# Kernel tuning notes

Hardware: AMD Instinct MI355X
Metric: run time of the kernel (lower is better)

## Reference

```python
import jax, jax.numpy as jnp
import numpy as np

N = 100000      # nodes
E = 1000000     # edges
G = 1024        # graphs
NODE_IN, CLIMBER_IN, HID, OUT, HEADS = 6, 4, 64, 4, 2
SLOPE = 0.2     # PyG GATConv default negative_slope


def gat_conv(x, edge_index, W, att_src, att_dst, bias):
    """PyG GATConv, heads=HEADS, concat=False (mean over heads), add_self_loops=True."""
    heads, ch = att_src.shape
    xp = (x @ W).reshape(-1, heads, ch)                       # [N,H,C]
    a_src = jnp.einsum('nhc,hc->nh', xp, att_src)             # [N,H]
    a_dst = jnp.einsum('nhc,hc->nh', xp, att_dst)
    loops = jnp.arange(x.shape[0])
    src = jnp.concatenate([edge_index[0], loops])             # [E+N]
    dst = jnp.concatenate([edge_index[1], loops])
    e = jax.nn.leaky_relu(a_src[src] + a_dst[dst], SLOPE)     # [E+N,H]
    emax = jax.ops.segment_max(e, dst, num_segments=x.shape[0])
    emax = jnp.where(jnp.isfinite(emax), emax, 0.0)
    ex = jnp.exp(e - emax[dst])
    den = jax.ops.segment_sum(ex, dst, num_segments=x.shape[0])
    alpha = ex / (den[dst] + 1e-16)                           # segment softmax over incoming edges
    msg = xp[src] * alpha[:, :, None]                         # [E+N,H,C]
    agg = jax.ops.segment_sum(msg, dst, num_segments=x.shape[0])  # [N,H,C]
    return agg.mean(axis=1) + bias                            # concat=False -> head mean


def setup_inputs() -> dict:
    key = jax.random.key(0)
    ks = jax.random.split(key, 20)
    s = lambda *d: 1.0 / np.sqrt(d[0])
    inp = {
        'x': jax.random.normal(ks[0], (N, NODE_IN), jnp.float32),
        'edge_index': jax.random.randint(ks[1], (2, E), 0, N),
        'batch': jnp.sort(jax.random.randint(ks[2], (N,), 0, G)),
        'climber': jax.random.normal(ks[3], (G, CLIMBER_IN), jnp.float32),
        # conv1 params
        'W1': jax.random.normal(ks[4], (NODE_IN, HEADS * HID), jnp.float32) * s(NODE_IN),
        'as1': jax.random.normal(ks[5], (HEADS, HID), jnp.float32) * s(HID),
        'ad1': jax.random.normal(ks[6], (HEADS, HID), jnp.float32) * s(HID),
        'b1': jnp.zeros((HID,), jnp.float32),
        # conv2 params
        'W2': jax.random.normal(ks[7], (HID, HEADS * HID), jnp.float32) * s(HID),
        'as2': jax.random.normal(ks[8], (HEADS, HID), jnp.float32) * s(HID),
        'ad2': jax.random.normal(ks[9], (HEADS, HID), jnp.float32) * s(HID),
        'b2': jnp.zeros((HID,), jnp.float32),
        # climber embed
        'Wc': jax.random.normal(ks[10], (CLIMBER_IN, HID), jnp.float32) * s(CLIMBER_IN),
        'bc': jnp.zeros((HID,), jnp.float32),
        # classifier
        'Wm1': jax.random.normal(ks[11], (2 * HID, HID), jnp.float32) * s(2 * HID),
        'bm1': jnp.zeros((HID,), jnp.float32),
        'Wm2': jax.random.normal(ks[12], (HID, OUT), jnp.float32) * s(HID),
        'bm2': jnp.zeros((OUT,), jnp.float32),
    }
    return inp


def reference(x, edge_index, batch, climber, W1, as1, ad1, b1, W2, as2, ad2, b2,
              Wc, bc, Wm1, bm1, Wm2, bm2):
    h = jax.nn.relu(gat_conv(x, edge_index, W1, as1, ad1, b1))
    h = jax.nn.relu(gat_conv(h, edge_index, W2, as2, ad2, b2))
    c = jax.nn.relu(climber @ Wc + bc)            # dropout is identity in eval mode
    z = jnp.concatenate([h, c[batch]], axis=1)    # [N, 2*HID]
    z = jax.nn.relu(z @ Wm1 + bm1)                # dropout identity (eval)
    return z @ Wm2 + bm2                          # [N, OUT]
```

## Files before the change

### kernel.cpp

```cpp
#include <hip/hip_runtime.h>
#include <hip/hip_fp16.h>

#define SLOPE 0.2f

__device__ __forceinline__ float lrelu(float v) { return v >= 0.f ? v : SLOPE * v; }

__device__ __forceinline__ unsigned pack2(float a, float b) {
    __half2 h = __floats2half2_rn(a, b);
    return *reinterpret_cast<unsigned*>(&h);
}

__device__ __forceinline__ void mix8(float4& A, float4& B, float a, uint4 u) {
    asm("v_fma_mix_f32 %0, %8, %12, %0 op_sel:[0,0,0] op_sel_hi:[1,0,0]\n\t"
        "v_fma_mix_f32 %1, %8, %12, %1 op_sel:[1,0,0] op_sel_hi:[1,0,0]\n\t"
        "v_fma_mix_f32 %2, %9, %12, %2 op_sel:[0,0,0] op_sel_hi:[1,0,0]\n\t"
        "v_fma_mix_f32 %3, %9, %12, %3 op_sel:[1,0,0] op_sel_hi:[1,0,0]\n\t"
        "v_fma_mix_f32 %4, %10, %12, %4 op_sel:[0,0,0] op_sel_hi:[1,0,0]\n\t"
        "v_fma_mix_f32 %5, %10, %12, %5 op_sel:[1,0,0] op_sel_hi:[1,0,0]\n\t"
        "v_fma_mix_f32 %6, %11, %12, %6 op_sel:[0,0,0] op_sel_hi:[1,0,0]\n\t"
        "v_fma_mix_f32 %7, %11, %12, %7 op_sel:[1,0,0] op_sel_hi:[1,0,0]"
        : "+v"(A.x), "+v"(A.y), "+v"(A.z), "+v"(A.w),
          "+v"(B.x), "+v"(B.y), "+v"(B.z), "+v"(B.w)
        : "v"(u.x), "v"(u.y), "v"(u.z), "v"(u.w), "v"(a));
}

template <int K>
__global__ __launch_bounds__(256)
void k_xp_gemm(const float* __restrict__ x, const float* __restrict__ W,
               const float* __restrict__ as_, const float* __restrict__ ad_,
               __half* __restrict__ xph, float* __restrict__ asrc,
               float* __restrict__ adst, int N) {
    constexpr int ZS = K + 1;
    __shared__ float zs[64 * ZS];
    __shared__ float ws[K * 128];
    const int n0 = blockIdx.x * 64;
    const int t = threadIdx.x;

    for (int i = t; i < K * 32; i += 256) ((float4*)ws)[i] = ((const float4*)W)[i];
    if constexpr (K % 4 == 0) {
        constexpr int K4 = K / 4;
        for (int i = t; i < 64 * K4; i += 256) {
            int n = i / K4, k4 = i - n * K4;
            int gn = n0 + n;
            float4 v = (gn < N) ? ((const float4*)x)[(size_t)gn * K4 + k4]
                                : make_float4(0.f, 0.f, 0.f, 0.f);
            float* zr = zs + n * ZS + k4 * 4;
            zr[0] = v.x; zr[1] = v.y; zr[2] = v.z; zr[3] = v.w;
        }
    } else {
        for (int i = t; i < 64 * K; i += 256) {
            int n = i / K, k = i - n * K;
            int gn = n0 + n;
            zs[n * ZS + k] = (gn < N) ? x[(size_t)gn * K + k] : 0.f;
        }
    }
    __syncthreads();

    const int tx = t & 15, ty = t >> 4;
    const int c0a = tx * 4;
    const int c0b = 64 + tx * 4;

    float4 asA = *(const float4*)(as_ + c0a);
    float4 asB = *(const float4*)(as_ + c0b);
    float4 adA = *(const float4*)(ad_ + c0a);
    float4 adB = *(const float4*)(ad_ + c0b);

    float acc[4][8];
    #pragma unroll
    for (int i = 0; i < 4; ++i)
        #pragma unroll
        for (int j = 0; j < 8; ++j) acc[i][j] = 0.f;

    for (int k = 0; k < K; ++k) {
        float4 w0 = *(const float4*)(ws + k * 128 + c0a);
        float4 w1 = *(const float4*)(ws + k * 128 + c0b);
        #pragma unroll
        for (int i = 0; i < 4; ++i) {
            float zv = zs[(ty * 4 + i) * ZS + k];
            acc[i][0] += zv * w0.x; acc[i][1] += zv * w0.y;
            acc[i][2] += zv * w0.z; acc[i][3] += zv * w0.w;
            acc[i][4] += zv * w1.x; acc[i][5] += zv * w1.y;
            acc[i][6] += zv * w1.z; acc[i][7] += zv * w1.w;
        }
    }

    #pragma unroll
    for (int i = 0; i < 4; ++i) {
        int nl = ty * 4 + i, gn = n0 + nl;
        if (gn < N) {
            uint2 ua, ub;
            ua.x = pack2(acc[i][0], acc[i][1]);
            ua.y = pack2(acc[i][2], acc[i][3]);
            ub.x = pack2(acc[i][4], acc[i][5]);
            ub.y = pack2(acc[i][6], acc[i][7]);
            *(uint2*)(xph + (size_t)gn * 128 + c0a) = ua;
            *(uint2*)(xph + (size_t)gn * 128 + c0b) = ub;
        }
        float ps0 = acc[i][0]*asA.x + acc[i][1]*asA.y + acc[i][2]*asA.z + acc[i][3]*asA.w;
        float ps1 = acc[i][4]*asB.x + acc[i][5]*asB.y + acc[i][6]*asB.z + acc[i][7]*asB.w;
        float pd0 = acc[i][0]*adA.x + acc[i][1]*adA.y + acc[i][2]*adA.z + acc[i][3]*adA.w;
        float pd1 = acc[i][4]*adB.x + acc[i][5]*adB.y + acc[i][6]*adB.z + acc[i][7]*adB.w;
        #pragma unroll
        for (int off = 1; off <= 8; off <<= 1) {
            ps0 += __shfl_xor(ps0, off, 64);
            ps1 += __shfl_xor(ps1, off, 64);
            pd0 += __shfl_xor(pd0, off, 64);
            pd1 += __shfl_xor(pd1, off, 64);
        }
        if (tx == 0 && gn < N) {
            asrc[gn * 2]     = ps0;
            asrc[gn * 2 + 1] = ps1;
            adst[gn * 2]     = pd0;
            adst[gn * 2 + 1] = pd1;
        }
    }
}

__global__ void k_hist(const int* __restrict__ dst, int* __restrict__ deg,
                       int* __restrict__ rank, int E) {
    int e = blockIdx.x * blockDim.x + threadIdx.x;
    if (e < E) rank[e] = atomicAdd(&deg[dst[e]], 1);
}

__global__ void k_scan_partial(const int* __restrict__ deg, int* __restrict__ partial, int N) {
    int b = blockIdx.x, t = threadIdx.x;
    int base = b * 1024 + t * 4;
    int s = 0;
    for (int i = 0; i < 4; ++i) { int idx = base + i; if (idx < N) s += deg[idx]; }
    __shared__ int sh[256];
    sh[t] = s; __syncthreads();
    for (int off = 128; off > 0; off >>= 1) { if (t < off) sh[t] += sh[t + off]; __syncthreads(); }
    if (t == 0) partial[b] = sh[0];
}

__global__ void k_scan_final(const int* __restrict__ deg, const int* __restrict__ partial,
                             int* __restrict__ rowptr, int N, int E, int nb) {
    int b = blockIdx.x, t = threadIdx.x;
    __shared__ int shp[256];
    shp[t] = (t < nb) ? partial[t] : 0;
    __syncthreads();
    for (int off = 1; off < 256; off <<= 1) {
        int v = (t >= off) ? shp[t - off] : 0;
        __syncthreads();
        shp[t] += v;
        __syncthreads();
    }
    int pbase = (b > 0) ? shp[b - 1] : 0;
    __syncthreads();

    int base = b * 1024 + t * 4;
    int local[4]; int s = 0;
    for (int i = 0; i < 4; ++i) { int idx = base + i; local[i] = (idx < N) ? deg[idx] : 0; s += local[i]; }
    __shared__ int sh[256];
    int orig = s;
    sh[t] = s; __syncthreads();
    for (int off = 1; off < 256; off <<= 1) {
        int v = (t >= off) ? sh[t - off] : 0;
        __syncthreads();
        sh[t] += v;
        __syncthreads();
    }
    int run = pbase + sh[t] - orig;
    for (int i = 0; i < 4; ++i) {
        int idx = base + i;
        if (idx < N) rowptr[idx] = run;
        run += local[i];
    }
    if (b == 0 && t == 0) rowptr[N] = E;
}

__global__ void k_scatter(const int* __restrict__ src, const int* __restrict__ dst,
                          const int* __restrict__ rowptr, const int* __restrict__ rank,
                          int* __restrict__ csr_src, int E) {
    int e = blockIdx.x * blockDim.x + threadIdx.x;
    if (e >= E) return;
    int d = dst[e];
    csr_src[rowptr[d] + rank[e]] = src[e];
}

__global__ void k_ag(const int* __restrict__ rowptr, const int* __restrict__ csr_src,
                     const float* __restrict__ asrc, const float* __restrict__ adst,
                     const __half* __restrict__ xph, const float* __restrict__ b,
                     float* __restrict__ hout, int N) {
    int tid = blockIdx.x * blockDim.x + threadIdx.x;
    int lane = threadIdx.x & 63;
    int wid = tid >> 6;
    int nw = (gridDim.x * blockDim.x) >> 6;
    const int l  = lane & 31;
    const int hh = lane >> 5;
    const int g4 = (lane >> 3) & 3;
    const int c8 = lane & 7;
    const int lofs = hh * 8 + c8;
    const uint4* xp4 = (const uint4*)xph;
    float4 bb0 = ((const float4*)b)[c8 * 2];
    float4 bb1 = ((const float4*)b)[c8 * 2 + 1];

    for (int n = wid; n < N; n += nw) {
        int rs = rowptr[n], re = rowptr[n + 1], cnt = re - rs;
        uint4 uself = xp4[(size_t)n * 16 + lofs];
        float a_dst = adst[n * 2 + hh];
        float eself = __expf(lrelu(asrc[n * 2 + hh] + a_dst));

        float4 accA = make_float4(0.f, 0.f, 0.f, 0.f);
        float4 accB = make_float4(0.f, 0.f, 0.f, 0.f);
        float den;

        if (cnt <= 32) {
            float ev = 0.f; int s_reg = n;
            if (l < cnt) {
                s_reg = csr_src[rs + l];
                ev = __expf(lrelu(asrc[s_reg * 2 + hh] + a_dst));
            }
            if (g4 == 0) mix8(accA, accB, eself, uself);

            const int base = (hh << 5) - rs;
            int e0 = rs;
            for (; e0 + 4 < re; e0 += 8) {
                int ea = e0 + g4, eb = e0 + 4 + g4;
                float aa = __shfl(ev,    base + ea, 64);
                int   sa = __shfl(s_reg, base + ea, 64);
                float ab = __shfl(ev,    base + eb, 64);
                int   sb = __shfl(s_reg, base + eb, 64);
                if (eb >= re) { ab = 0.f; sb = n; }
                uint4 u1 = xp4[(size_t)sa * 16 + lofs];
                uint4 u2 = xp4[(size_t)sb * 16 + lofs];
                mix8(accA, accB, aa, u1);
                mix8(accA, accB, ab, u2);
            }
            if (e0 < re) {
                int ea = e0 + g4;
                float aa = __shfl(ev,    base + ea, 64);
                int   sa = __shfl(s_reg, base + ea, 64);
                if (ea >= re) { aa = 0.f; sa = n; }
                uint4 u1 = xp4[(size_t)sa * 16 + lofs];
                mix8(accA, accB, aa, u1);
            }
            den = ev + (l == 0 ? eself : 0.f);
            #pragma unroll
            for (int off = 16; off > 0; off >>= 1) den += __shfl_xor(den, off, 64);
        } else {
            den = (l == 0) ? eself : 0.f;
            for (int e = rs + l; e < re; e += 32)
                den += __expf(lrelu(asrc[csr_src[e] * 2 + hh] + a_dst));
            #pragma unroll
            for (int off = 16; off > 0; off >>= 1) den += __shfl_xor(den, off, 64);
            if (g4 == 0) mix8(accA, accB, eself, uself);
            for (int e0 = rs; e0 < re; e0 += 8) {
                int ea = e0 + g4, eb = e0 + 4 + g4;
                bool va = ea < re, vb = eb < re;
                int sa = va ? csr_src[ea] : n;
                int sb = vb ? csr_src[eb] : n;
                float aa = va ? __expf(lrelu(asrc[sa * 2 + hh] + a_dst)) : 0.f;
                float ab = vb ? __expf(lrelu(asrc[sb * 2 + hh] + a_dst)) : 0.f;
                uint4 u1 = xp4[(size_t)sa * 16 + lofs];
                uint4 u2 = xp4[(size_t)sb * 16 + lofs];
                mix8(accA, accB, aa, u1);
                mix8(accA, accB, ab, u2);
            }
        }

        float inv = 1.f / (den + 1e-16f);

        #pragma unroll
        for (int off = 8; off <= 16; off <<= 1) {
            accA.x += __shfl_xor(accA.x, off, 64);
            accA.y += __shfl_xor(accA.y, off, 64);
            accA.z += __shfl_xor(accA.z, off, 64);
            accA.w += __shfl_xor(accA.w, off, 64);
            accB.x += __shfl_xor(accB.x, off, 64);
            accB.y += __shfl_xor(accB.y, off, 64);
            accB.z += __shfl_xor(accB.z, off, 64);
            accB.w += __shfl_xor(accB.w, off, 64);
        }
        accA.x *= inv; accA.y *= inv; accA.z *= inv; accA.w *= inv;
        accB.x *= inv; accB.y *= inv; accB.z *= inv; accB.w *= inv;
        accA.x += __shfl_xor(accA.x, 32, 64);
        accA.y += __shfl_xor(accA.y, 32, 64);
        accA.z += __shfl_xor(accA.z, 32, 64);
        accA.w += __shfl_xor(accA.w, 32, 64);
        accB.x += __shfl_xor(accB.x, 32, 64);
        accB.y += __shfl_xor(accB.y, 32, 64);
        accB.z += __shfl_xor(accB.z, 32, 64);
        accB.w += __shfl_xor(accB.w, 32, 64);

        if (lane < 8) {
            float4 r0, r1;
            r0.x = fmaxf(accA.x * 0.5f + bb0.x, 0.f);
            r0.y = fmaxf(accA.y * 0.5f + bb0.y, 0.f);
            r0.z = fmaxf(accA.z * 0.5f + bb0.z, 0.f);
            r0.w = fmaxf(accA.w * 0.5f + bb0.w, 0.f);
            r1.x = fmaxf(accB.x * 0.5f + bb1.x, 0.f);
            r1.y = fmaxf(accB.y * 0.5f + bb1.y, 0.f);
            r1.z = fmaxf(accB.z * 0.5f + bb1.z, 0.f);
            r1.w = fmaxf(accB.w * 0.5f + bb1.w, 0.f);
            ((float4*)hout)[(size_t)n * 16 + c8 * 2]     = r0;
            ((float4*)hout)[(size_t)n * 16 + c8 * 2 + 1] = r1;
        }
    }
}

__global__ __launch_bounds__(256)
void k_climber_cpre(const float* __restrict__ climber, const float* __restrict__ Wc,
                    const float* __restrict__ bc, const float* __restrict__ Wm1,
                    const float* __restrict__ bm1, float* __restrict__ cpre, int G) {
    __shared__ float ce[4][64];
    __shared__ float wm1b[64 * 64];
    int t = threadIdx.x;
    for (int i = t; i < 1024; i += 256) ((float4*)wm1b)[i] = ((const float4*)Wm1)[1024 + i];
    int gl = t >> 6, c = t & 63;
    int g = blockIdx.x * 4 + gl;
    float acc = bc[c];
    if (g < G)
        for (int k = 0; k < 4; ++k) acc += climber[g * 4 + k] * Wc[k * 64 + c];
    ce[gl][c] = fmaxf(acc, 0.f);
    __syncthreads();
    float o = bm1[c];
    for (int k = 0; k < 64; ++k) o += ce[gl][k] * wm1b[k * 64 + c];
    if (g < G) cpre[(size_t)g * 64 + c] = o;
}

__global__ __launch_bounds__(256)
void k_final(const float* __restrict__ h2, const float* __restrict__ cpre,
             const int* __restrict__ batch, const float* __restrict__ Wm1,
             const float* __restrict__ Wm2, const float* __restrict__ bm2,
             float* __restrict__ out, int N) {
    __shared__ float zs[64 * 65];
    __shared__ float ws[64 * 64];
    __shared__ float4 w2l[64];
    const int n0 = blockIdx.x * 64;
    const int t = threadIdx.x;

    for (int i = t; i < 1024; i += 256) ((float4*)ws)[i] = ((const float4*)Wm1)[i];
    if (t < 64) w2l[t] = ((const float4*)Wm2)[t];
    for (int i = t; i < 64 * 16; i += 256) {
        int n = i >> 4, k4 = i & 15;
        int gn = n0 + n;
        float4 v = (gn < N) ? ((const float4*)h2)[(size_t)gn * 16 + k4]
                            : make_float4(0.f, 0.f, 0.f, 0.f);
        float* zr = zs + n * 65 + k4 * 4;
        zr[0] = v.x; zr[1] = v.y; zr[2] = v.z; zr[3] = v.w;
    }
    __syncthreads();

    const int tx = t & 15, ty = t >> 4;
    const int c0 = tx * 4;
    float acc[4][4];
    #pragma unroll
    for (int i = 0; i < 4; ++i)
        #pragma unroll
        for (int j = 0; j < 4; ++j) acc[i][j] = 0.f;

    for (int k = 0; k < 64; ++k) {
        float4 wv = *(const float4*)(ws + k * 64 + c0);
        #pragma unroll
        for (int i = 0; i < 4; ++i) {
            float zv = zs[(ty * 4 + i) * 65 + k];
            acc[i][0] += zv * wv.x; acc[i][1] += zv * wv.y;
            acc[i][2] += zv * wv.z; acc[i][3] += zv * wv.w;
        }
    }
    __syncthreads();

    float4 wa = w2l[c0], wb = w2l[c0 + 1], wc = w2l[c0 + 2], wd = w2l[c0 + 3];
    #pragma unroll
    for (int i = 0; i < 4; ++i) {
        int nl = ty * 4 + i, gn = n0 + nl;
        float4 o = make_float4(0.f, 0.f, 0.f, 0.f);
        if (gn < N) {
            int b = batch[gn];
            float4 cp = *(const float4*)(cpre + (size_t)b * 64 + c0);
            float m0 = fmaxf(acc[i][0] + cp.x, 0.f);
            float m1 = fmaxf(acc[i][1] + cp.y, 0.f);
            float m2 = fmaxf(acc[i][2] + cp.z, 0.f);
            float m3 = fmaxf(acc[i][3] + cp.w, 0.f);
            o.x = m0 * wa.x + m1 * wb.x + m2 * wc.x + m3 * wd.x;
            o.y = m0 * wa.y + m1 * wb.y + m2 * wc.y + m3 * wd.y;
            o.z = m0 * wa.z + m1 * wb.z + m2 * wc.z + m3 * wd.z;
            o.w = m0 * wa.w + m1 * wb.w + m2 * wc.w + m3 * wd.w;
        }
        *(float4*)(zs + tx * 260 + nl * 4) = o;
    }
    __syncthreads();
    {
        int nl = t >> 2, j = t & 3, gn = n0 + nl;
        float s = 0.f;
        #pragma unroll
        for (int tx2 = 0; tx2 < 16; ++tx2) s += zs[tx2 * 260 + nl * 4 + j];
        if (gn < N) out[(size_t)gn * 4 + j] = s + bm2[j];
    }
}

extern "C" void kernel_launch(void* const* d_in, const int* in_sizes, int n_in,
                              void* d_out, int out_size, void* d_ws, size_t ws_size,
                              hipStream_t stream) {
    const float* x       = (const float*)d_in[0];
    const int*   ei      = (const int*)  d_in[1];
    const int*   batch   = (const int*)  d_in[2];
    const float* climber = (const float*)d_in[3];
    const float* W1  = (const float*)d_in[4];
    const float* as1 = (const float*)d_in[5];
    const float* ad1 = (const float*)d_in[6];
    const float* b1  = (const float*)d_in[7];
    const float* W2  = (const float*)d_in[8];
    const float* as2 = (const float*)d_in[9];
    const float* ad2 = (const float*)d_in[10];
    const float* b2  = (const float*)d_in[11];
    const float* Wc  = (const float*)d_in[12];
    const float* bc  = (const float*)d_in[13];
    const float* Wm1 = (const float*)d_in[14];
    const float* bm1 = (const float*)d_in[15];
    const float* Wm2 = (const float*)d_in[16];
    const float* bm2 = (const float*)d_in[17];

    const int N  = in_sizes[0] / 6;
    const int E  = in_sizes[1] / 2;
    const int G  = in_sizes[3] / 4;

    const int* srcI = ei;
    const int* dstI = ei + E;

    char* base = (char*)d_ws;
    size_t off = 0;
    auto carve = [&](size_t bytes) { void* p = base + off; off += (bytes + 255) & ~size_t(255); return p; };
    __half* xph   = (__half*)carve((size_t)N * 128 * 2);
    float* hbuf   = (float*)carve((size_t)N * 64 * 4);
    float* asrc   = (float*)carve((size_t)N * 2 * 4);
    float* adst   = (float*)carve((size_t)N * 2 * 4);
    float* cpre   = (float*)carve((size_t)G * 64 * 4);
    int*   deg    = (int*)  carve((size_t)N * 4);
    int*   rowptr = (int*)  carve((size_t)(N + 1) * 4);
    int*   rank   = (int*)  carve((size_t)E * 4);
    int*   partial= (int*)  carve(4096 * 4);
    int*   csr_src= (int*)  carve((size_t)E * 4);

    const int tpb = 256;
    const int nScanBlk = (N + 1023) / 1024;
    const int nEdgeBlk = (E + tpb - 1) / tpb;
    const int PG = 2048;
    const int nTile = (N + 63) / 64;

    hipMemsetAsync(deg, 0, (size_t)N * 4, stream);
    k_hist<<<nEdgeBlk, tpb, 0, stream>>>(dstI, deg, rank, E);
    k_scan_partial<<<nScanBlk, tpb, 0, stream>>>(deg, partial, N);
    k_scan_final<<<nScanBlk, tpb, 0, stream>>>(deg, partial, rowptr, N, E, nScanBlk);
    k_scatter<<<nEdgeBlk, tpb, 0, stream>>>(srcI, dstI, rowptr, rank, csr_src, E);

    k_xp_gemm<6><<<nTile, tpb, 0, stream>>>(x, W1, as1, ad1, xph, asrc, adst, N);
    k_ag<<<PG, tpb, 0, stream>>>(rowptr, csr_src, asrc, adst, xph, b1, hbuf, N);

    k_xp_gemm<64><<<nTile, tpb, 0, stream>>>(hbuf, W2, as2, ad2, xph, asrc, adst, N);
    k_ag<<<PG, tpb, 0, stream>>>(rowptr, csr_src, asrc, adst, xph, b2, hbuf, N);

    k_climber_cpre<<<(G + 3) / 4, tpb, 0, stream>>>(climber, Wc, bc, Wm1, bm1, cpre, G);
    k_final<<<nTile, tpb, 0, stream>>>(hbuf, cpre, batch, Wm1, Wm2, bm2, (float*)d_out, N);
}
```

Measured before the change: 330.0 us.

## Software-pipeline per-node loads in GAT aggregation with contiguous node chunks

The aggregation kernel now gives each wavefront a contiguous chunk of nodes instead of a grid-strided set. It loads the chunk's row pointers once across lanes and reads them back with shuffles. While the current node is being aggregated, it prefetches the next node's CSR indices, self features and attention scalars, and loads the next node's source attention values after the current gather. The aim is to hide the dependent load latency at the start of each node, at the cost of more live registers and some load imbalance between wavefronts with different chunk contents.

```diff
diff --git a/kernel.cpp b/kernel.cpp
--- a/kernel.cpp
+++ b/kernel.cpp
@@ -195,32 +195,67 @@
     float4 bb0 = ((const float4*)b)[c8 * 2];
     float4 bb1 = ((const float4*)b)[c8 * 2 + 1];
 
-    for (int n = wid; n < N; n += nw) {
-        int rs = rowptr[n], re = rowptr[n + 1], cnt = re - rs;
-        uint4 uself = xp4[(size_t)n * 16 + lofs];
-        float a_dst = adst[n * 2 + hh];
-        float eself = __expf(lrelu(asrc[n * 2 + hh] + a_dst));
-
+    const int cpw = (N + nw - 1) / nw;
+    const int nb = wid * cpw;
+    if (nb >= N) return;
+    const int ne = min(N, nb + cpw);
+    const bool use_rp = (cpw <= 62);
+
+    int rpv = 0;
+    if (use_rp) {
+        int gi = nb + lane;
+        rpv = (gi <= ne) ? rowptr[gi] : 0;
+    }
+
+    int rs, re;
+    if (use_rp) { rs = __shfl(rpv, 0, 64); re = __shfl(rpv, 1, 64); }
+    else        { rs = rowptr[nb];         re = rowptr[nb + 1]; }
+    int cnt = re - rs;
+    int   s_cur = nb;
+    float a_cur = 0.f;
+    if (cnt <= 32 && l < cnt) {
+        s_cur = csr_src[rs + l];
+        a_cur = asrc[s_cur * 2 + hh];
+    }
+    uint4 u_self = xp4[(size_t)nb * 16 + lofs];
+    float asel   = asrc[nb * 2 + hh];
+    float adv    = adst[nb * 2 + hh];
+
+    for (int n = nb; n < ne; ++n) {
+        const int i = n - nb;
+        const int n1 = n + 1;
+        const bool has1 = n1 < ne;
+
+        int rs1 = 0, re1 = 0, cnt1 = 0, s_nxt = n1;
+        uint4 u_nxt = make_uint4(0u, 0u, 0u, 0u);
+        float asel_nxt = 0.f, adv_nxt = 0.f;
+        if (has1) {
+            if (use_rp) { rs1 = __shfl(rpv, i + 1, 64); re1 = __shfl(rpv, i + 2, 64); }
+            else        { rs1 = rowptr[n1];             re1 = rowptr[n1 + 1]; }
+            cnt1 = re1 - rs1;
+            if (cnt1 <= 32 && l < cnt1) s_nxt = csr_src[rs1 + l];
+            u_nxt    = xp4[(size_t)n1 * 16 + lofs];
+            asel_nxt = asrc[n1 * 2 + hh];
+            adv_nxt  = adst[n1 * 2 + hh];
+        }
+
+        float eself = __expf(lrelu(asel + adv));
         float4 accA = make_float4(0.f, 0.f, 0.f, 0.f);
         float4 accB = make_float4(0.f, 0.f, 0.f, 0.f);
         float den;
 
         if (cnt <= 32) {
-            float ev = 0.f; int s_reg = n;
-            if (l < cnt) {
-                s_reg = csr_src[rs + l];
-                ev = __expf(lrelu(asrc[s_reg * 2 + hh] + a_dst));
-            }
-            if (g4 == 0) mix8(accA, accB, eself, uself);
+            float ev = (l < cnt) ? __expf(lrelu(a_cur + adv)) : 0.f;
+            if (g4 == 0) mix8(accA, accB, eself, u_self);
 
             const int base = (hh << 5) - rs;
             int e0 = rs;
             for (; e0 + 4 < re; e0 += 8) {
                 int ea = e0 + g4, eb = e0 + 4 + g4;
                 float aa = __shfl(ev,    base + ea, 64);
-                int   sa = __shfl(s_reg, base + ea, 64);
+                int   sa = __shfl(s_cur, base + ea, 64);
                 float ab = __shfl(ev,    base + eb, 64);
-                int   sb = __shfl(s_reg, base + eb, 64);
+                int   sb = __shfl(s_cur, base + eb, 64);
                 if (eb >= re) { ab = 0.f; sb = n; }
                 uint4 u1 = xp4[(size_t)sa * 16 + lofs];
                 uint4 u2 = xp4[(size_t)sb * 16 + lofs];
@@ -230,7 +265,7 @@
             if (e0 < re) {
                 int ea = e0 + g4;
                 float aa = __shfl(ev,    base + ea, 64);
-                int   sa = __shfl(s_reg, base + ea, 64);
+                int   sa = __shfl(s_cur, base + ea, 64);
                 if (ea >= re) { aa = 0.f; sa = n; }
                 uint4 u1 = xp4[(size_t)sa * 16 + lofs];
                 mix8(accA, accB, aa, u1);
@@ -241,23 +276,26 @@
         } else {
             den = (l == 0) ? eself : 0.f;
             for (int e = rs + l; e < re; e += 32)
-                den += __expf(lrelu(asrc[csr_src[e] * 2 + hh] + a_dst));
+                den += __expf(lrelu(asrc[csr_src[e] * 2 + hh] + adv));
             #pragma unroll
             for (int off = 16; off > 0; off >>= 1) den += __shfl_xor(den, off, 64);
-            if (g4 == 0) mix8(accA, accB, eself, uself);
+            if (g4 == 0) mix8(accA, accB, eself, u_self);
             for (int e0 = rs; e0 < re; e0 += 8) {
                 int ea = e0 + g4, eb = e0 + 4 + g4;
                 bool va = ea < re, vb = eb < re;
                 int sa = va ? csr_src[ea] : n;
                 int sb = vb ? csr_src[eb] : n;
-                float aa = va ? __expf(lrelu(asrc[sa * 2 + hh] + a_dst)) : 0.f;
-                float ab = vb ? __expf(lrelu(asrc[sb * 2 + hh] + a_dst)) : 0.f;
+                float aa = va ? __expf(lrelu(asrc[sa * 2 + hh] + adv)) : 0.f;
+                float ab = vb ? __expf(lrelu(asrc[sb * 2 + hh] + adv)) : 0.f;
                 uint4 u1 = xp4[(size_t)sa * 16 + lofs];
                 uint4 u2 = xp4[(size_t)sb * 16 + lofs];
                 mix8(accA, accB, aa, u1);
                 mix8(accA, accB, ab, u2);
             }
         }
+
+        float a_nxt = 0.f;
+        if (has1 && cnt1 <= 32 && l < cnt1) a_nxt = asrc[s_nxt * 2 + hh];
 
         float inv = 1.f / (den + 1e-16f);
 
@@ -296,6 +334,10 @@
             ((float4*)hout)[(size_t)n * 16 + c8 * 2]     = r0;
             ((float4*)hout)[(size_t)n * 16 + c8 * 2 + 1] = r1;
         }
+
+        rs = rs1; re = re1; cnt = cnt1;
+        s_cur = s_nxt; a_cur = a_nxt;
+        u_self = u_nxt; asel = asel_nxt; adv = adv_nxt;
     }
 }
 
```

After: 367.8 us. 1.11x slower.

## Fuse scatter, layer-1 projection and climber kernels; store hidden activations in fp16

Applied to the files above, without the earlier changes.

Merges the CSR scatter, the first-layer projection GEMM and the climber precompute into one launch, dispatching on block index, so three independent kernels run concurrently and two launches disappear. The intermediate hidden buffer between layers is now stored as fp16 instead of fp32, which halves its write and read traffic in the aggregation, second GEMM and final kernels. The cost is reduced precision on the hidden activations and a larger, branchier fused kernel whose shared-memory footprint is sized for the largest branch.

```diff
diff --git a/kernel.cpp b/kernel.cpp
--- a/kernel.cpp
+++ b/kernel.cpp
@@ -8,6 +8,10 @@
 __device__ __forceinline__ unsigned pack2(float a, float b) {
     __half2 h = __floats2half2_rn(a, b);
     return *reinterpret_cast<unsigned*>(&h);
+}
+__device__ __forceinline__ float2 h2f(unsigned u) {
+    __half2 h = *reinterpret_cast<__half2*>(&u);
+    return __half22float2(h);
 }
 
 __device__ __forceinline__ void mix8(float4& A, float4& B, float a, uint4 u) {
@@ -24,12 +28,12 @@
         : "v"(u.x), "v"(u.y), "v"(u.z), "v"(u.w), "v"(a));
 }
 
-template <int K>
 __global__ __launch_bounds__(256)
-void k_xp_gemm(const float* __restrict__ x, const float* __restrict__ W,
-               const float* __restrict__ as_, const float* __restrict__ ad_,
-               __half* __restrict__ xph, float* __restrict__ asrc,
-               float* __restrict__ adst, int N) {
+void k_xp_gemm64h(const __half* __restrict__ x, const float* __restrict__ W,
+                  const float* __restrict__ as_, const float* __restrict__ ad_,
+                  __half* __restrict__ xph, float* __restrict__ asrc,
+                  float* __restrict__ adst, int N) {
+    constexpr int K = 64;
     constexpr int ZS = K + 1;
     __shared__ float zs[64 * ZS];
     __shared__ float ws[K * 128];
@@ -37,22 +41,15 @@
     const int t = threadIdx.x;
 
     for (int i = t; i < K * 32; i += 256) ((float4*)ws)[i] = ((const float4*)W)[i];
-    if constexpr (K % 4 == 0) {
-        constexpr int K4 = K / 4;
-        for (int i = t; i < 64 * K4; i += 256) {
-            int n = i / K4, k4 = i - n * K4;
-            int gn = n0 + n;
-            float4 v = (gn < N) ? ((const float4*)x)[(size_t)gn * K4 + k4]
-                                : make_float4(0.f, 0.f, 0.f, 0.f);
-            float* zr = zs + n * ZS + k4 * 4;
-            zr[0] = v.x; zr[1] = v.y; zr[2] = v.z; zr[3] = v.w;
-        }
-    } else {
-        for (int i = t; i < 64 * K; i += 256) {
-            int n = i / K, k = i - n * K;
-            int gn = n0 + n;
-            zs[n * ZS + k] = (gn < N) ? x[(size_t)gn * K + k] : 0.f;
-        }
+    for (int i = t; i < 64 * 8; i += 256) {
+        int n = i >> 3, k8 = i & 7;
+        int gn = n0 + n;
+        uint4 v = make_uint4(0u, 0u, 0u, 0u);
+        if (gn < N) v = ((const uint4*)x)[(size_t)gn * 8 + k8];
+        float2 f0 = h2f(v.x), f1 = h2f(v.y), f2 = h2f(v.z), f3 = h2f(v.w);
+        float* zr = zs + n * ZS + k8 * 8;
+        zr[0] = f0.x; zr[1] = f0.y; zr[2] = f1.x; zr[3] = f1.y;
+        zr[4] = f2.x; zr[5] = f2.y; zr[6] = f3.x; zr[7] = f3.y;
     }
     __syncthreads();
 
@@ -169,19 +166,127 @@
     if (b == 0 && t == 0) rowptr[N] = E;
 }
 
-__global__ void k_scatter(const int* __restrict__ src, const int* __restrict__ dst,
-                          const int* __restrict__ rowptr, const int* __restrict__ rank,
-                          int* __restrict__ csr_src, int E) {
-    int e = blockIdx.x * blockDim.x + threadIdx.x;
-    if (e >= E) return;
-    int d = dst[e];
-    csr_src[rowptr[d] + rank[e]] = src[e];
+__global__ __launch_bounds__(256)
+void k_fused3(const int* __restrict__ srcI, const int* __restrict__ dstI,
+              const int* __restrict__ rowptr, const int* __restrict__ rank,
+              int* __restrict__ csr_src, int E,
+              const float* __restrict__ x, const float* __restrict__ W1,
+              const float* __restrict__ as1, const float* __restrict__ ad1,
+              __half* __restrict__ xph, float* __restrict__ asrc,
+              float* __restrict__ adst, int N,
+              const float* __restrict__ climber, const float* __restrict__ Wc,
+              const float* __restrict__ bc, const float* __restrict__ Wm1,
+              const float* __restrict__ bm1, float* __restrict__ cpre, int G,
+              int nEdgeBlk, int nTile) {
+    __shared__ float smem[4352];
+    int bid = blockIdx.x;
+    const int t = threadIdx.x;
+
+    if (bid < nEdgeBlk) {
+        int e = bid * 256 + t;
+        if (e < E) {
+            int d = dstI[e];
+            csr_src[rowptr[d] + rank[e]] = srcI[e];
+        }
+        return;
+    }
+    bid -= nEdgeBlk;
+    if (bid < nTile) {
+        constexpr int K = 6, ZS = 7;
+        float* zs = smem;
+        float* ws = smem + 448;
+        const int n0 = bid * 64;
+
+        for (int i = t; i < K * 32; i += 256) ((float4*)ws)[i] = ((const float4*)W1)[i];
+        for (int i = t; i < 64 * K; i += 256) {
+            int n = i / K, k = i - n * K;
+            int gn = n0 + n;
+            zs[n * ZS + k] = (gn < N) ? x[(size_t)gn * K + k] : 0.f;
+        }
+        __syncthreads();
+
+        const int tx = t & 15, ty = t >> 4;
+        const int c0a = tx * 4;
+        const int c0b = 64 + tx * 4;
+
+        float4 asA = *(const float4*)(as1 + c0a);
+        float4 asB = *(const float4*)(as1 + c0b);
+        float4 adA = *(const float4*)(ad1 + c0a);
+        float4 adB = *(const float4*)(ad1 + c0b);
+
+        float acc[4][8];
+        #pragma unroll
+        for (int i = 0; i < 4; ++i)
+            #pragma unroll
+            for (int j = 0; j < 8; ++j) acc[i][j] = 0.f;
+
+        for (int k = 0; k < K; ++k) {
+            float4 w0 = *(const float4*)(ws + k * 128 + c0a);
+            float4 w1 = *(const float4*)(ws + k * 128 + c0b);
+            #pragma unroll
+            for (int i = 0; i < 4; ++i) {
+                float zv = zs[(ty * 4 + i) * ZS + k];
+                acc[i][0] += zv * w0.x; acc[i][1] += zv * w0.y;
+                acc[i][2] += zv * w0.z; acc[i][3] += zv * w0.w;
+                acc[i][4] += zv * w1.x; acc[i][5] += zv * w1.y;
+                acc[i][6] += zv * w1.z; acc[i][7] += zv * w1.w;
+            }
+        }
+
+        #pragma unroll
+        for (int i = 0; i < 4; ++i) {
+            int nl = ty * 4 + i, gn = n0 + nl;
+            if (gn < N) {
+                uint2 ua, ub;
+                ua.x = pack2(acc[i][0], acc[i][1]);
+                ua.y = pack2(acc[i][2], acc[i][3]);
+                ub.x = pack2(acc[i][4], acc[i][5]);
+                ub.y = pack2(acc[i][6], acc[i][7]);
+                *(uint2*)(xph + (size_t)gn * 128 + c0a) = ua;
+                *(uint2*)(xph + (size_t)gn * 128 + c0b) = ub;
+            }
+            float ps0 = acc[i][0]*asA.x + acc[i][1]*asA.y + acc[i][2]*asA.z + acc[i][3]*asA.w;
+            float ps1 = acc[i][4]*asB.x + acc[i][5]*asB.y + acc[i][6]*asB.z + acc[i][7]*asB.w;
+            float pd0 = acc[i][0]*adA.x + acc[i][1]*adA.y + acc[i][2]*adA.z + acc[i][3]*adA.w;
+            float pd1 = acc[i][4]*adB.x + acc[i][5]*adB.y + acc[i][6]*adB.z + acc[i][7]*adB.w;
+            #pragma unroll
+            for (int off = 1; off <= 8; off <<= 1) {
+                ps0 += __shfl_xor(ps0, off, 64);
+                ps1 += __shfl_xor(ps1, off, 64);
+                pd0 += __shfl_xor(pd0, off, 64);
+                pd1 += __shfl_xor(pd1, off, 64);
+            }
+            if (tx == 0 && gn < N) {
+                asrc[gn * 2]     = ps0;
+                asrc[gn * 2 + 1] = ps1;
+                adst[gn * 2]     = pd0;
+                adst[gn * 2 + 1] = pd1;
+            }
+        }
+        return;
+    }
+    bid -= nTile;
+    {
+        float* ce   = smem;
+        float* wm1b = smem + 256;
+        for (int i = t; i < 1024; i += 256) ((float4*)wm1b)[i] = ((const float4*)Wm1)[1024 + i];
+        int gl = t >> 6, c = t & 63;
+        int g = bid * 4 + gl;
+        float acc = bc[c];
+        if (g < G)
+            for (int k = 0; k < 4; ++k) acc += climber[g * 4 + k] * Wc[k * 64 + c];
+        ce[gl * 64 + c] = fmaxf(acc, 0.f);
+        __syncthreads();
+        float o = bm1[c];
+        for (int k = 0; k < 64; ++k) o += ce[gl * 64 + k] * wm1b[k * 64 + c];
+        if (g < G) cpre[(size_t)g * 64 + c] = o;
+    }
 }
 
 __global__ void k_ag(const int* __restrict__ rowptr, const int* __restrict__ csr_src,
                      const float* __restrict__ asrc, const float* __restrict__ adst,
                      const __half* __restrict__ xph, const float* __restrict__ b,
-                     float* __restrict__ hout, int N) {
+                     __half* __restrict__ hout, int N) {
     int tid = blockIdx.x * blockDim.x + threadIdx.x;
     int lane = threadIdx.x & 63;
     int wid = tid >> 6;
@@ -284,43 +389,22 @@
         accB.w += __shfl_xor(accB.w, 32, 64);
 
         if (lane < 8) {
-            float4 r0, r1;
-            r0.x = fmaxf(accA.x * 0.5f + bb0.x, 0.f);
-            r0.y = fmaxf(accA.y * 0.5f + bb0.y, 0.f);
-            r0.z = fmaxf(accA.z * 0.5f + bb0.z, 0.f);
-            r0.w = fmaxf(accA.w * 0.5f + bb0.w, 0.f);
-            r1.x = fmaxf(accB.x * 0.5f + bb1.x, 0.f);
-            r1.y = fmaxf(accB.y * 0.5f + bb1.y, 0.f);
-            r1.z = fmaxf(accB.z * 0.5f + bb1.z, 0.f);
-            r1.w = fmaxf(accB.w * 0.5f + bb1.w, 0.f);
-            ((float4*)hout)[(size_t)n * 16 + c8 * 2]     = r0;
-            ((float4*)hout)[(size_t)n * 16 + c8 * 2 + 1] = r1;
+            uint4 up;
+            up.x = pack2(fmaxf(accA.x * 0.5f + bb0.x, 0.f),
+                         fmaxf(accA.y * 0.5f + bb0.y, 0.f));
+            up.y = pack2(fmaxf(accA.z * 0.5f + bb0.z, 0.f),
+                         fmaxf(accA.w * 0.5f + bb0.w, 0.f));
+            up.z = pack2(fmaxf(accB.x * 0.5f + bb1.x, 0.f),
+                         fmaxf(accB.y * 0.5f + bb1.y, 0.f));
+            up.w = pack2(fmaxf(accB.z * 0.5f + bb1.z, 0.f),
+                         fmaxf(accB.w * 0.5f + bb1.w, 0.f));
+            ((uint4*)hout)[(size_t)n * 8 + c8] = up;
         }
     }
 }
 
 __global__ __launch_bounds__(256)
-void k_climber_cpre(const float* __restrict__ climber, const float* __restrict__ Wc,
-                    const float* __restrict__ bc, const float* __restrict__ Wm1,
-                    const float* __restrict__ bm1, float* __restrict__ cpre, int G) {
-    __shared__ float ce[4][64];
-    __shared__ float wm1b[64 * 64];
-    int t = threadIdx.x;
-    for (int i = t; i < 1024; i += 256) ((float4*)wm1b)[i] = ((const float4*)Wm1)[1024 + i];
-    int gl = t >> 6, c = t & 63;
-    int g = blockIdx.x * 4 + gl;
-    float acc = bc[c];
-    if (g < G)
-        for (int k = 0; k < 4; ++k) acc += climber[g * 4 + k] * Wc[k * 64 + c];
-    ce[gl][c] = fmaxf(acc, 0.f);
-    __syncthreads();
-    float o = bm1[c];
-    for (int k = 0; k < 64; ++k) o += ce[gl][k] * wm1b[k * 64 + c];
-    if (g < G) cpre[(size_t)g * 64 + c] = o;
-}
-
-__global__ __launch_bounds__(256)
-void k_final(const float* __restrict__ h2, const float* __restrict__ cpre,
+void k_final(const __half* __restrict__ h2, const float* __restrict__ cpre,
              const int* __restrict__ batch, const float* __restrict__ Wm1,
              const float* __restrict__ Wm2, const float* __restrict__ bm2,
              float* __restrict__ out, int N) {
@@ -332,13 +416,15 @@
 
     for (int i = t; i < 1024; i += 256) ((float4*)ws)[i] = ((const float4*)Wm1)[i];
     if (t < 64) w2l[t] = ((const float4*)Wm2)[t];
-    for (int i = t; i < 64 * 16; i += 256) {
-        int n = i >> 4, k4 = i & 15;
+    for (int i = t; i < 64 * 8; i += 256) {
+        int n = i >> 3, k8 = i & 7;
         int gn = n0 + n;
-        float4 v = (gn < N) ? ((const float4*)h2)[(size_t)gn * 16 + k4]
-                            : make_float4(0.f, 0.f, 0.f, 0.f);
-        float* zr = zs + n * 65 + k4 * 4;
-        zr[0] = v.x; zr[1] = v.y; zr[2] = v.z; zr[3] = v.w;
+        uint4 v = make_uint4(0u, 0u, 0u, 0u);
+        if (gn < N) v = ((const uint4*)h2)[(size_t)gn * 8 + k8];
+        float2 f0 = h2f(v.x), f1 = h2f(v.y), f2 = h2f(v.z), f3 = h2f(v.w);
+        float* zr = zs + n * 65 + k8 * 8;
+        zr[0] = f0.x; zr[1] = f0.y; zr[2] = f1.x; zr[3] = f1.y;
+        zr[4] = f2.x; zr[5] = f2.y; zr[6] = f3.x; zr[7] = f3.y;
     }
     __syncthreads();
 
@@ -423,7 +509,7 @@
     size_t off = 0;
     auto carve = [&](size_t bytes) { void* p = base + off; off += (bytes + 255) & ~size_t(255); return p; };
     __half* xph   = (__half*)carve((size_t)N * 128 * 2);
-    float* hbuf   = (float*)carve((size_t)N * 64 * 4);
+    __half* hbuf  = (__half*)carve((size_t)N * 64 * 2);
     float* asrc   = (float*)carve((size_t)N * 2 * 4);
     float* adst   = (float*)carve((size_t)N * 2 * 4);
     float* cpre   = (float*)carve((size_t)G * 64 * 4);
@@ -436,6 +522,7 @@
     const int tpb = 256;
     const int nScanBlk = (N + 1023) / 1024;
     const int nEdgeBlk = (E + tpb - 1) / tpb;
+    const int nClimber = (G + 3) / 4;
     const int PG = 2048;
     const int nTile = (N + 63) / 64;
 
@@ -443,14 +530,15 @@
     k_hist<<<nEdgeBlk, tpb, 0, stream>>>(dstI, deg, rank, E);
     k_scan_partial<<<nScanBlk, tpb, 0, stream>>>(deg, partial, N);
     k_scan_final<<<nScanBlk, tpb, 0, stream>>>(deg, partial, rowptr, N, E, nScanBlk);
-    k_scatter<<<nEdgeBlk, tpb, 0, stream>>>(srcI, dstI, rowptr, rank, csr_src, E);
-
-    k_xp_gemm<6><<<nTile, tpb, 0, stream>>>(x, W1, as1, ad1, xph, asrc, adst, N);
+    k_fused3<<<nEdgeBlk + nTile + nClimber, tpb, 0, stream>>>(
+        srcI, dstI, rowptr, rank, csr_src, E,
+        x, W1, as1, ad1, xph, asrc, adst, N,
+        climber, Wc, bc, Wm1, bm1, cpre, G, nEdgeBlk, nTile);
+
     k_ag<<<PG, tpb, 0, stream>>>(rowptr, csr_src, asrc, adst, xph, b1, hbuf, N);
 
-    k_xp_gemm<64><<<nTile, tpb, 0, stream>>>(hbuf, W2, as2, ad2, xph, asrc, adst, N);
+    k_xp_gemm64h<<<nTile, tpb, 0, stream>>>(hbuf, W2, as2, ad2, xph, asrc, adst, N);
     k_ag<<<PG, tpb, 0, stream>>>(rowptr, csr_src, asrc, adst, xph, b2, hbuf, N);
 
-    k_climber_cpre<<<(G + 3) / 4, tpb, 0, stream>>>(climber, Wc, bc, Wm1, bm1, cpre, G);
     k_final<<<nTile, tpb, 0, stream>>>(hbuf, cpre, batch, Wm1, Wm2, bm2, (float*)d_out, N);
 }
```

Result: faster. 318.0 us (-3.7%).
